# Kernel optimization log

Measured on AMD Instinct MI355X. Metric: run time of the kernel, lower is better.

Reference implementation:

```python
import jax, jax.numpy as jnp
import numpy as np

HIDDEN = 2048
N_HEADS = 32
N_KV = 8
HEAD_DIM = HIDDEN // N_HEADS  # 64
GROUP = N_HEADS // N_KV       # 4
FFN = 8192
EPS = 1e-5
ROPE_BASE = 500000.0
NEG = -1e9


def rms_norm(x, w, eps=EPS):
    var = jnp.mean(x * x, axis=-1, keepdims=True)
    return x * jax.lax.rsqrt(var + eps) * w


def rope_cos_sin(position_ids):
    # inv_freq: [head_dim//2]
    inv_freq = 1.0 / (ROPE_BASE ** (jnp.arange(0, HEAD_DIM, 2, dtype=jnp.float32) / HEAD_DIM))
    freqs = position_ids.astype(jnp.float32)[:, :, None] * inv_freq[None, None, :]  # [b,s,d/2]
    emb = jnp.concatenate([freqs, freqs], axis=-1)  # [b,s,d]
    return jnp.cos(emb), jnp.sin(emb)


def rotate_half(x):
    x1, x2 = jnp.split(x, 2, axis=-1)
    return jnp.concatenate([-x2, x1], axis=-1)


def setup_inputs() -> dict:
    key = jax.random.key(0)
    ks = jax.random.split(key, 12)
    b, s = 2, 1024
    scale_h = 1.0 / np.sqrt(HIDDEN)
    scale_f = 1.0 / np.sqrt(FFN)
    hidden_states = jax.random.normal(ks[0], (b, s, HIDDEN), jnp.float32)
    causal = jnp.where(jnp.tril(jnp.ones((s, s), bool)), 0.0, NEG).astype(jnp.float32)
    attention_mask = jnp.broadcast_to(causal[None, None], (b, 1, s, s))
    position_ids = jnp.broadcast_to(jnp.arange(s, dtype=jnp.int32)[None], (b, s))
    return {
        "hidden_states": hidden_states,
        "attention_mask": attention_mask,
        "wq": jax.random.normal(ks[1], (HIDDEN, N_HEADS * HEAD_DIM), jnp.float32) * scale_h,
        "wk": jax.random.normal(ks[2], (HIDDEN, N_KV * HEAD_DIM), jnp.float32) * scale_h,
        "wv": jax.random.normal(ks[3], (HIDDEN, N_KV * HEAD_DIM), jnp.float32) * scale_h,
        "wo": jax.random.normal(ks[4], (N_HEADS * HEAD_DIM, HIDDEN), jnp.float32) * scale_h,
        "norm1_w": jnp.ones((HIDDEN,), jnp.float32),
        "norm2_w": jnp.ones((HIDDEN,), jnp.float32),
        "w_gate": jax.random.normal(ks[5], (HIDDEN, FFN), jnp.float32) * scale_h,
        "w_up": jax.random.normal(ks[6], (HIDDEN, FFN), jnp.float32) * scale_h,
        "w_down": jax.random.normal(ks[7], (FFN, HIDDEN), jnp.float32) * scale_f,
        "position_ids": position_ids,
    }


def reference(hidden_states, attention_mask, wq, wk, wv, wo, norm1_w, norm2_w,
              w_gate, w_up, w_down, position_ids):
    b, s, _ = hidden_states.shape
    residual = hidden_states
    normed = rms_norm(hidden_states, norm1_w)

    q = (normed @ wq).reshape(b, s, N_HEADS, HEAD_DIM).transpose(0, 2, 1, 3)  # [b,H,s,d]
    k = (normed @ wk).reshape(b, s, N_KV, HEAD_DIM).transpose(0, 2, 1, 3)    # [b,G,s,d]
    v = (normed @ wv).reshape(b, s, N_KV, HEAD_DIM).transpose(0, 2, 1, 3)

    cos, sin = rope_cos_sin(position_ids)  # [b,s,d]
    cos, sin = cos[:, None], sin[:, None]  # unsqueeze head dim
    q = q * cos + rotate_half(q) * sin
    k = k * cos + rotate_half(k) * sin

    # repeat_kv: [b,G,s,d] -> [b,H,s,d]
    k = jnp.repeat(k, GROUP, axis=1)
    v = jnp.repeat(v, GROUP, axis=1)

    scores = jnp.einsum('bhqd,bhkd->bhqk', q, k)
    scores = scores + attention_mask  # mask added BEFORE scaling, as in source
    attn = jax.nn.softmax(scores / np.sqrt(HEAD_DIM), axis=-1)
    ctx = jnp.einsum('bhqk,bhkd->bhqd', attn, v)
    ctx = ctx.transpose(0, 2, 1, 3).reshape(b, s, N_HEADS * HEAD_DIM)
    attn_out = ctx @ wo

    normed_ff = rms_norm(attn_out + residual, norm2_w)
    ff = (jax.nn.silu(normed_ff @ w_gate) * (normed_ff @ w_up)) @ w_down
    return attn_out + ff
```

## Files before the change

kernel.cpp:

```cpp
#include <hip/hip_runtime.h>
#include <hip/hip_bf16.h>
#include <cstddef>
#include <cstdint>

#define T_TOK   2048
#define HID     2048
#define NHEADS  32
#define NKV     8
#define HDIM    64
#define FFN_DIM 8192
#define QKV_N   3072

typedef __hip_bfloat16 bf16;
typedef __attribute__((ext_vector_type(8))) short short8;
typedef __attribute__((ext_vector_type(4))) float f32x4;
typedef __attribute__((ext_vector_type(4))) unsigned short us4;

typedef __attribute__((address_space(1))) const void cg_void;
typedef __attribute__((address_space(3))) void lds_void;

__global__ __launch_bounds__(256) void cast_transpose(const float* __restrict__ in,
                                                      bf16* __restrict__ out,
                                                      int K, int N)
{
    __shared__ bf16 t[64][65];
    const int n0 = blockIdx.x * 64, k0 = blockIdx.y * 64;
    const int tn = threadIdx.x & 63, tk = threadIdx.x >> 6;
    #pragma unroll
    for (int kk = tk; kk < 64; kk += 4)
        t[kk][tn] = __float2bfloat16(in[(size_t)(k0 + kk) * N + n0 + tn]);
    __syncthreads();
    #pragma unroll
    for (int nn = tk; nn < 64; nn += 4)
        out[(size_t)(n0 + nn) * K + k0 + tn] = t[tn][nn];
}

__global__ __launch_bounds__(256) void cast_ilv(const float* __restrict__ in,
                                                bf16* __restrict__ out,
                                                int N, int is_up)
{
    __shared__ bf16 t[64][65];
    const int n0 = blockIdx.x * 64, k0 = blockIdx.y * 64;
    const int tn = threadIdx.x & 63, tk = threadIdx.x >> 6;
    #pragma unroll
    for (int kk = tk; kk < 64; kk += 4)
        t[kk][tn] = __float2bfloat16(in[(size_t)(k0 + kk) * N + n0 + tn]);
    __syncthreads();
    #pragma unroll
    for (int nn = tk; nn < 64; nn += 4) {
        int n = n0 + nn;
        int r = ((n >> 5) << 6) + (is_up << 5) + (n & 31);
        out[(size_t)r * HID + k0 + tn] = t[tn][nn];
    }
}

__global__ __launch_bounds__(256) void rmsnorm_kernel(const float* __restrict__ x,
                                                      const float* __restrict__ w,
                                                      bf16* __restrict__ out)
{
    __shared__ float sm[4];
    const int row = blockIdx.x, tid = threadIdx.x;
    const float4* xr = (const float4*)(x + (size_t)row * HID);
    float4 a = xr[tid], b = xr[tid + 256];
    float ss = a.x*a.x + a.y*a.y + a.z*a.z + a.w*a.w
             + b.x*b.x + b.y*b.y + b.z*b.z + b.w*b.w;
    #pragma unroll
    for (int off = 32; off; off >>= 1) ss += __shfl_down(ss, off);
    if ((tid & 63) == 0) sm[tid >> 6] = ss;
    __syncthreads();
    float sc = rsqrtf((sm[0] + sm[1] + sm[2] + sm[3]) * (1.0f / HID) + 1e-5f);
    const float4* wr = (const float4*)w;
    float4 w0 = wr[tid], w1 = wr[tid + 256];
    bf16* o = out + (size_t)row * HID;
    o[tid*4+0] = __float2bfloat16(a.x * sc * w0.x);
    o[tid*4+1] = __float2bfloat16(a.y * sc * w0.y);
    o[tid*4+2] = __float2bfloat16(a.z * sc * w0.z);
    o[tid*4+3] = __float2bfloat16(a.w * sc * w0.w);
    o[1024+tid*4+0] = __float2bfloat16(b.x * sc * w1.x);
    o[1024+tid*4+1] = __float2bfloat16(b.y * sc * w1.y);
    o[1024+tid*4+2] = __float2bfloat16(b.z * sc * w1.z);
    o[1024+tid*4+3] = __float2bfloat16(b.w * sc * w1.w);
}

__global__ __launch_bounds__(256) void rmsnorm_add_kernel(const float* __restrict__ xa,
                                                          const float* __restrict__ xb,
                                                          const float* __restrict__ w,
                                                          bf16* __restrict__ out)
{
    __shared__ float sm[4];
    const int row = blockIdx.x, tid = threadIdx.x;
    const float4* ar = (const float4*)(xa + (size_t)row * HID);
    const float4* br = (const float4*)(xb + (size_t)row * HID);
    float4 a0 = ar[tid], a1 = ar[tid + 256];
    float4 b0 = br[tid], b1 = br[tid + 256];
    float4 s0, s1;
    s0.x = a0.x + b0.x; s0.y = a0.y + b0.y; s0.z = a0.z + b0.z; s0.w = a0.w + b0.w;
    s1.x = a1.x + b1.x; s1.y = a1.y + b1.y; s1.z = a1.z + b1.z; s1.w = a1.w + b1.w;
    float ss = s0.x*s0.x + s0.y*s0.y + s0.z*s0.z + s0.w*s0.w
             + s1.x*s1.x + s1.y*s1.y + s1.z*s1.z + s1.w*s1.w;
    #pragma unroll
    for (int off = 32; off; off >>= 1) ss += __shfl_down(ss, off);
    if ((tid & 63) == 0) sm[tid >> 6] = ss;
    __syncthreads();
    float sc = rsqrtf((sm[0] + sm[1] + sm[2] + sm[3]) * (1.0f / HID) + 1e-5f);
    const float4* wr = (const float4*)w;
    float4 w0 = wr[tid], w1 = wr[tid + 256];
    bf16* o = out + (size_t)row * HID;
    o[tid*4+0] = __float2bfloat16(s0.x * sc * w0.x);
    o[tid*4+1] = __float2bfloat16(s0.y * sc * w0.y);
    o[tid*4+2] = __float2bfloat16(s0.z * sc * w0.z);
    o[tid*4+3] = __float2bfloat16(s0.w * sc * w0.w);
    o[1024+tid*4+0] = __float2bfloat16(s1.x * sc * w1.x);
    o[1024+tid*4+1] = __float2bfloat16(s1.y * sc * w1.y);
    o[1024+tid*4+2] = __float2bfloat16(s1.z * sc * w1.z);
    o[1024+tid*4+3] = __float2bfloat16(s1.w * sc * w1.w);
}

template<int BN, int EPI>
__device__ __forceinline__ void gemm_body(
    const bf16* __restrict__ A, const bf16* __restrict__ Bt,
    float* __restrict__ Cf, bf16* __restrict__ Cb,
    int lda, int kbeg, int klen, int ldc, int bx, int by)
{
    constexpr int NFR   = BN / 32;
    constexpr int CALLS = 4 + NFR;
    __shared__ bf16 As[2 * 128 * 64];
    __shared__ bf16 Bs[2 * BN * 64];
    const int tid = threadIdx.x;
    const int wv = tid >> 6, ln = tid & 63;
    const int wr = wv >> 1, wc = wv & 1;
    const size_t m0 = (size_t)by * 128;
    const size_t n0 = (size_t)bx * BN;

    const int lrow = ln >> 3;
    const int lk   = (ln & 7) ^ lrow;

    const bf16* Abase = A  + (m0 + (size_t)wv*32 + lrow) * lda + kbeg + lk*8;
    const bf16* Bbase = Bt + (n0 + (size_t)wv*NFR*8 + lrow) * lda + kbeg + lk*8;
    bf16* AsW = As + wv*2048;
    bf16* BsW = Bs + wv*NFR*512;

    auto stage = [&](int p, int tk) {
        #pragma unroll
        for (int i = 0; i < 4; ++i)
            __builtin_amdgcn_global_load_lds((cg_void*)(Abase + (size_t)i*8*lda + tk),
                                             (lds_void*)(AsW + p*8192 + i*512), 16, 0, 0);
        #pragma unroll
        for (int i = 0; i < NFR; ++i)
            __builtin_amdgcn_global_load_lds((cg_void*)(Bbase + (size_t)i*8*lda + tk),
                                             (lds_void*)(BsW + p*(BN*64) + i*512), 16, 0, 0);
    };

    f32x4 acc[4][NFR] = {};
    const int nt = klen >> 6;

    stage(0, 0);
    stage(1, 64);
    asm volatile("s_waitcnt vmcnt(%0)" :: "n"(CALLS) : "memory");
    __builtin_amdgcn_sched_barrier(0);
    __builtin_amdgcn_s_barrier();

    for (int t = 0; t < nt; ++t) {
        const int p = t & 1;
        const char* Ab = (const char*)As + p * 16384;
        const char* Bb = (const char*)Bs + p * (BN * 128);

        short8 af[4][2], bfr[NFR][2];
        #pragma unroll
        for (int ks = 0; ks < 2; ++ks) {
            const int kbyte = ks*64 + (ln >> 4)*16;
            #pragma unroll
            for (int m = 0; m < 4; ++m) {
                int row = wr*64 + m*16 + (ln & 15);
                af[m][ks] = *(const short8*)(Ab + row*128 + (kbyte ^ ((row & 7) << 4)));
            }
            #pragma unroll
            for (int n = 0; n < NFR; ++n) {
                int row = wc*(BN/2) + n*16 + (ln & 15);
                bfr[n][ks] = *(const short8*)(Bb + row*128 + (kbyte ^ ((row & 7) << 4)));
            }
        }
        asm volatile("s_waitcnt lgkmcnt(0)" ::: "memory");
        __builtin_amdgcn_sched_barrier(0);
        __builtin_amdgcn_s_barrier();

        const bool more = (t + 2 < nt);
        if (more) stage(p, (t + 2) * 64);
        __builtin_amdgcn_sched_barrier(0);

        __builtin_amdgcn_s_setprio(1);
        #pragma unroll
        for (int ks = 0; ks < 2; ++ks)
            #pragma unroll
            for (int m = 0; m < 4; ++m)
                #pragma unroll
                for (int n = 0; n < NFR; ++n)
                    acc[m][n] = __builtin_amdgcn_mfma_f32_16x16x32_bf16(af[m][ks], bfr[n][ks], acc[m][n], 0, 0, 0);
        __builtin_amdgcn_s_setprio(0);

        if (more) { asm volatile("s_waitcnt vmcnt(%0)" :: "n"(CALLS) : "memory"); }
        else      { asm volatile("s_waitcnt vmcnt(0)" ::: "memory"); }
        __builtin_amdgcn_sched_barrier(0);
        __builtin_amdgcn_s_barrier();
    }

    const int cj = ln & 15, rj = ln >> 4;
    if constexpr (EPI == 4) {
        #pragma unroll
        for (int m = 0; m < 4; ++m) {
            #pragma unroll
            for (int j = 0; j < 4; ++j) {
                size_t row = m0 + wr*64 + m*16 + rj*4 + j;
                #pragma unroll
                for (int n = 0; n < 2; ++n) {
                    int col = ((int)(n0 >> 6) + wc) * 32 + n*16 + cj;
                    float g = acc[m][n][j];
                    float u = acc[m][n+2][j];
                    Cb[row * (size_t)ldc + col] =
                        __float2bfloat16(g / (1.0f + __expf(-g)) * u);
                }
            }
        }
    } else {
        #pragma unroll
        for (int m = 0; m < 4; ++m) {
            #pragma unroll
            for (int j = 0; j < 4; ++j) {
                size_t row = m0 + wr*64 + m*16 + rj*4 + j;
                #pragma unroll
                for (int n = 0; n < NFR; ++n) {
                    int col = (int)n0 + wc*(BN/2) + n*16 + cj;
                    float v = acc[m][n][j];
                    size_t off = row * (size_t)ldc + col;
                    if constexpr (EPI == 0) Cf[off] = v;
                    else if constexpr (EPI == 5) unsafeAtomicAdd(&Cf[off], v);
                }
            }
        }
    }
}

__device__ __forceinline__ void swz(int& bx, int& by) {
    const int nwg = gridDim.x * gridDim.y;
    int orig = blockIdx.y * gridDim.x + blockIdx.x;
    int wg = (orig & 7) * (nwg >> 3) + (orig >> 3);
    by = wg % gridDim.y;
    bx = wg / gridDim.y;
}

__global__ __launch_bounds__(256) void g_qkv(const bf16* __restrict__ A,
                                             const bf16* __restrict__ Bt,
                                             float* __restrict__ C) {
    int bx, by; swz(bx, by);
    gemm_body<64,0>(A, Bt, C, nullptr, HID, 0, HID, QKV_N, bx, by);
}
__global__ __launch_bounds__(256) void g_wo(const bf16* __restrict__ A,
                                            const bf16* __restrict__ Bt,
                                            float* __restrict__ C) {
    int bx, by; swz(bx, by);
    gemm_body<64,0>(A, Bt, C, nullptr, HID, 0, HID, HID, bx, by);
}
__global__ __launch_bounds__(256) void g_gateup(const bf16* __restrict__ A,
                                                const bf16* __restrict__ Bt,
                                                bf16* __restrict__ C) {
    int bx, by; swz(bx, by);
    gemm_body<128,4>(A, Bt, nullptr, C, HID, 0, HID, FFN_DIM, bx, by);
}
__global__ __launch_bounds__(256) void g_down(const bf16* __restrict__ A,
                                              const bf16* __restrict__ Bt,
                                              float* __restrict__ C) {
    int bx, by; swz(bx, by);
    gemm_body<64,5>(A, Bt, C, nullptr, FFN_DIM, blockIdx.z * 4096, 4096, HID, bx, by);
}

__global__ __launch_bounds__(256) void rope_cast(const float* __restrict__ qkv,
                                                 const int* __restrict__ pos_ids,
                                                 bf16* __restrict__ Qp,
                                                 bf16* __restrict__ Kp)
{
    const int t = blockIdx.x, tid = threadIdx.x;
    const int b = t >> 10, s = t & 1023;
    const float pos = (float)pos_ids[t];
    const float* row = qkv + (size_t)t * QKV_N;

    {
        int idx = tid * 4;
        int hq = idx >> 5, j = idx & 31;
        float xa[4], xb[4];
        *(float4*)xa = *(const float4*)(row + hq*64 + j);
        *(float4*)xb = *(const float4*)(row + hq*64 + j + 32);
        us4 o1, o2;
        #pragma unroll
        for (int jj = 0; jj < 4; ++jj) {
            float inv = exp2f(-(float)(j + jj) * 0.5916115177913804f);
            float ang = pos * inv, c, sn;
            sincosf(ang, &sn, &c);
            o1[jj] = __bfloat16_as_ushort(__float2bfloat16(xa[jj]*c - xb[jj]*sn));
            o2[jj] = __bfloat16_as_ushort(__float2bfloat16(xb[jj]*c + xa[jj]*sn));
        }
        bf16* qd = Qp + ((size_t)(b*32 + hq)*1024 + s)*64;
        *(us4*)(qd + j)      = o1;
        *(us4*)(qd + j + 32) = o2;
    }
    {
        int hk = tid >> 5, j = tid & 31;
        float a = row[2048 + hk*64 + j];
        float bb = row[2048 + hk*64 + j + 32];
        float inv = exp2f(-(float)j * 0.5916115177913804f);
        float ang = pos * inv, c, sn;
        sincosf(ang, &sn, &c);
        bf16* kd = Kp + ((size_t)(b*8 + hk)*1024 + s)*64;
        kd[j]      = __float2bfloat16(a*c - bb*sn);
        kd[j + 32] = __float2bfloat16(bb*c + a*sn);
    }
}

__global__ __launch_bounds__(256) void vt_cast(const float* __restrict__ qkv,
                                               bf16* __restrict__ Vt)
{
    __shared__ bf16 tile[64][64];
    const int s0 = blockIdx.x * 64;
    const int sec = blockIdx.y;
    const int b = sec >> 3, hk = sec & 7;
    const int tid = threadIdx.x;
    const float* base = qkv + ((size_t)(b*1024 + s0)) * QKV_N + 2560 + hk*64;
    const int srow = tid >> 2, d0 = (tid & 3) * 16;
    #pragma unroll
    for (int q = 0; q < 4; ++q) {
        float va[4];
        *(float4*)va = *(const float4*)(base + (size_t)srow * QKV_N + d0 + q*4);
        #pragma unroll
        for (int cc = 0; cc < 4; ++cc)
            tile[d0 + q*4 + cc][srow] = __float2bfloat16(va[cc]);
    }
    __syncthreads();
    const int dr = tid >> 2, sc = (tid & 3) * 16;
    bf16* od = Vt + ((size_t)sec*64 + dr)*1024 + s0 + sc;
    *(short8*)od       = *(const short8*)&tile[dr][sc];
    *(short8*)(od + 8) = *(const short8*)&tile[dr][sc + 8];
}

__global__ __launch_bounds__(256) void attn_mfma(const bf16* __restrict__ Qp,
                                                 const bf16* __restrict__ Kp,
                                                 const bf16* __restrict__ Vt,
                                                 bf16* __restrict__ ctx)
{
    __shared__ bf16 Ks[128 * 64];
    __shared__ bf16 Vs[64 * 128];
    __shared__ bf16 Ps[4 * 32 * 128];
    const int tid = threadIdx.x;
    const int w = tid >> 6, ln = tid & 63;
    const int qt = blockIdx.x, h = blockIdx.y, b = blockIdx.z;
    const int hk = h >> 2;
    const int q0 = qt * 128;

    const bf16* qsec = Qp + ((size_t)(b*32 + h)*1024 + q0 + w*32)*64;
    const bf16* ksec = Kp + ((size_t)(b*8 + hk)*1024)*64;
    const bf16* vsec = Vt + ((size_t)(b*8 + hk))*64*1024;

    short8 qf[2][2];
    #pragma unroll
    for (int f = 0; f < 2; ++f)
        #pragma unroll
        for (int kc = 0; kc < 2; ++kc)
            qf[f][kc] = *(const short8*)(qsec + (size_t)(f*16 + (ln & 15))*64 + kc*32 + (ln >> 4)*8);

    f32x4 acc_o[2][4] = {};
    f32x4 m[2], l[2];
    #pragma unroll
    for (int f = 0; f < 2; ++f)
        #pragma unroll
        for (int j = 0; j < 4; ++j) { m[f][j] = -1e30f; l[f][j] = 0.0f; }

    const int lrow = ln >> 3;
    const int lkk  = (ln & 7) ^ lrow;
    char* PsW = (char*)Ps + w * 8192;

    const int ntiles = qt + 1;
    for (int kt = 0; kt < ntiles; ++kt) {
        const int kv0 = kt * 128;
        {
            const bf16* kbase = ksec + (size_t)(kv0 + w*32 + lrow)*64 + lkk*8;
            bf16* KsW = Ks + w*2048;
            #pragma unroll
            for (int i = 0; i < 4; ++i)
                __builtin_amdgcn_global_load_lds((cg_void*)(kbase + (size_t)i*8*64),
                                                 (lds_void*)(KsW + i*512), 16, 0, 0);
        }
        {
            bf16* VsW = Vs + w*2048;
            #pragma unroll
            for (int i = 0; i < 4; ++i) {
                int d = w*16 + i*4 + (ln >> 4);
                __builtin_amdgcn_global_load_lds(
                    (cg_void*)(vsec + (size_t)d*1024 + kv0 + (((ln & 15) ^ (d & 7))*8)),
                    (lds_void*)(VsW + i*512), 16, 0, 0);
            }
        }
        __syncthreads();

        f32x4 acc_s[2][8] = {};
        #pragma unroll
        for (int c = 0; c < 8; ++c) {
            int kvr = c*16 + (ln & 15);
            const char* krow = (const char*)Ks + kvr*128;
            short8 kf0 = *(const short8*)(krow + (((ln >> 4)*16)      ^ ((kvr & 7) << 4)));
            short8 kf1 = *(const short8*)(krow + ((64 + (ln >> 4)*16) ^ ((kvr & 7) << 4)));
            #pragma unroll
            for (int f = 0; f < 2; ++f) {
                acc_s[f][c] = __builtin_amdgcn_mfma_f32_16x16x32_bf16(qf[f][0], kf0, acc_s[f][c], 0, 0, 0);
                acc_s[f][c] = __builtin_amdgcn_mfma_f32_16x16x32_bf16(qf[f][1], kf1, acc_s[f][c], 0, 0, 0);
            }
        }

        const bool diag = (kt == qt);
        f32x4 vmax[2];
        #pragma unroll
        for (int f = 0; f < 2; ++f)
            #pragma unroll
            for (int j = 0; j < 4; ++j) vmax[f][j] = -1e30f;
        #pragma unroll
        for (int f = 0; f < 2; ++f) {
            #pragma unroll
            for (int c = 0; c < 8; ++c) {
                f32x4 t = acc_s[f][c] * 0.125f;
                if (diag) {
                    int kv = kv0 + c*16 + (ln & 15);
                    int qg = q0 + w*32 + f*16 + (ln >> 4)*4;
                    #pragma unroll
                    for (int j = 0; j < 4; ++j)
                        if (kv > qg + j) t[j] = -1e30f;
                }
                acc_s[f][c] = t;
                #pragma unroll
                for (int j = 0; j < 4; ++j) vmax[f][j] = fmaxf(vmax[f][j], t[j]);
            }
            #pragma unroll
            for (int mk = 1; mk <= 8; mk <<= 1)
                #pragma unroll
                for (int j = 0; j < 4; ++j)
                    vmax[f][j] = fmaxf(vmax[f][j], __shfl_xor(vmax[f][j], mk));
        }

        #pragma unroll
        for (int f = 0; f < 2; ++f) {
            f32x4 r;
            #pragma unroll
            for (int j = 0; j < 4; ++j) {
                float mn = fmaxf(m[f][j], vmax[f][j]);
                r[j] = __expf(m[f][j] - mn);
                m[f][j] = mn;
                l[f][j] *= r[j];
            }
            #pragma unroll
            for (int df = 0; df < 4; ++df)
                #pragma unroll
                for (int j = 0; j < 4; ++j) acc_o[f][df][j] *= r[j];
        }

        f32x4 rs[2] = {};
        #pragma unroll
        for (int f = 0; f < 2; ++f) {
            #pragma unroll
            for (int c = 0; c < 8; ++c) {
                #pragma unroll
                for (int j = 0; j < 4; ++j) {
                    float p = __expf(acc_s[f][c][j] - m[f][j]);
                    rs[f][j] += p;
                    int qloc = f*16 + (ln >> 4)*4 + j;
                    int kvb  = (c*16 + (ln & 15))*2;
                    *(bf16*)(PsW + qloc*256 + (kvb ^ ((qloc & 7) << 4))) = __float2bfloat16(p);
                }
            }
            #pragma unroll
            for (int mk = 1; mk <= 8; mk <<= 1)
                #pragma unroll
                for (int j = 0; j < 4; ++j)
                    rs[f][j] += __shfl_xor(rs[f][j], mk);
            #pragma unroll
            for (int j = 0; j < 4; ++j) l[f][j] += rs[f][j];
        }

        #pragma unroll
        for (int kc = 0; kc < 4; ++kc) {
            short8 pa[2];
            #pragma unroll
            for (int f = 0; f < 2; ++f) {
                int qloc = f*16 + (ln & 15);
                pa[f] = *(const short8*)(PsW + qloc*256 + ((kc*64 + (ln >> 4)*16) ^ ((qloc & 7) << 4)));
            }
            #pragma unroll
            for (int df = 0; df < 4; ++df) {
                int dl = df*16 + (ln & 15);
                short8 vfr = *(const short8*)((const char*)Vs + dl*256 + ((kc*64 + (ln >> 4)*16) ^ ((dl & 7) << 4)));
                #pragma unroll
                for (int f = 0; f < 2; ++f)
                    acc_o[f][df] = __builtin_amdgcn_mfma_f32_16x16x32_bf16(pa[f], vfr, acc_o[f][df], 0, 0, 0);
            }
        }
        __syncthreads();
    }

    #pragma unroll
    for (int f = 0; f < 2; ++f) {
        f32x4 inv;
        #pragma unroll
        for (int j = 0; j < 4; ++j) inv[j] = 1.0f / l[f][j];
        #pragma unroll
        for (int df = 0; df < 4; ++df) {
            #pragma unroll
            for (int j = 0; j < 4; ++j) {
                int q = q0 + w*32 + f*16 + (ln >> 4)*4 + j;
                int d = df*16 + (ln & 15);
                ctx[((size_t)b*1024 + q)*HID + h*64 + d] = __float2bfloat16(acc_o[f][df][j] * inv[j]);
            }
        }
    }
}

extern "C" void kernel_launch(void* const* d_in, const int* in_sizes, int n_in,
                              void* d_out, int out_size, void* d_ws, size_t ws_size,
                              hipStream_t stream)
{
    const float* hidden = (const float*)d_in[0];
    const float* wq = (const float*)d_in[2];
    const float* wk = (const float*)d_in[3];
    const float* wv = (const float*)d_in[4];
    const float* wo = (const float*)d_in[5];
    const float* n1 = (const float*)d_in[6];
    const float* n2 = (const float*)d_in[7];
    const float* wg = (const float*)d_in[8];
    const float* wu = (const float*)d_in[9];
    const float* wd = (const float*)d_in[10];
    const int*  pos = (const int*)d_in[11];
    float* out = (float*)d_out;
    char* ws = (char*)d_ws;

    bf16* wgu_t  = (bf16*)(ws + 0);
    bf16* wd_t   = (bf16*)(ws + 67108864);
    bf16* wqkv_t = (bf16*)(ws + 100663296);
    bf16* wo_t   = (bf16*)(ws + 113246208);
    bf16* normed = (bf16*)(ws + 121634816);
    float* qkv   = (float*)(ws + 130023424);
    bf16* ctx    = (bf16*)(ws + 155189248);
    bf16* hb     = (bf16*)(ws + 130023424);
    bf16* Qp     = (bf16*)(ws + 121634816);
    bf16* Kp     = (bf16*)(ws + 163577856);
    bf16* Vt     = (bf16*)(ws + 165675008);

    cast_transpose<<<dim3(32, 32), 256, 0, stream>>>(wq, wqkv_t, 2048, 2048);
    cast_transpose<<<dim3(8, 32),  256, 0, stream>>>(wk, wqkv_t + 4194304, 2048, 512);
    cast_transpose<<<dim3(8, 32),  256, 0, stream>>>(wv, wqkv_t + 5242880, 2048, 512);
    cast_transpose<<<dim3(32, 32), 256, 0, stream>>>(wo, wo_t, 2048, 2048);
    cast_ilv<<<dim3(128, 32), 256, 0, stream>>>(wg, wgu_t, FFN_DIM, 0);
    cast_ilv<<<dim3(128, 32), 256, 0, stream>>>(wu, wgu_t, FFN_DIM, 1);
    cast_transpose<<<dim3(32, 128),256, 0, stream>>>(wd, wd_t, 8192, 2048);

    rmsnorm_kernel<<<T_TOK, 256, 0, stream>>>(hidden, n1, normed);
    g_qkv<<<dim3(QKV_N/64, T_TOK/128), 256, 0, stream>>>(normed, wqkv_t, qkv);
    rope_cast<<<T_TOK, 256, 0, stream>>>(qkv, pos, Qp, Kp);
    vt_cast<<<dim3(16, 16), 256, 0, stream>>>(qkv, Vt);
    attn_mfma<<<dim3(8, NHEADS, 2), 256, 0, stream>>>(Qp, Kp, Vt, ctx);
    g_wo<<<dim3(HID/64, T_TOK/128), 256, 0, stream>>>(ctx, wo_t, out);
    rmsnorm_add_kernel<<<T_TOK, 256, 0, stream>>>(out, hidden, n2, normed);
    g_gateup<<<dim3(16384/128, T_TOK/128), 256, 0, stream>>>(normed, wgu_t, hb);
    g_down<<<dim3(HID/64, T_TOK/128, 2), 256, 0, stream>>>(hb, wd_t, out);
}
```

Before: 539.9 us.

## Use dedicated 256x256 tile, 512-thread kernel for gate/up GEMM

Replaces the shared 128x128, 256-thread gate/up GEMM with a dedicated kernel that computes 256x256 output tiles using 8 waves, each owning a 128x64 sub-tile. Each LDS load of A and B is reused across more MFMAs, which cuts global and LDS traffic per flop for the largest GEMM in the layer. The cost is more accumulator registers (128 floats per lane) with a launch_bounds of 512,2, which risks spills or lower occupancy. The grid shrinks to 64x8 workgroups, which may leave some CUs with uneven load. The generic gemm_body loses its bf16 SwiGLU epilogue, which is now inlined in the new kernel.

```diff
diff --git a/kernel.cpp b/kernel.cpp
--- a/kernel.cpp
+++ b/kernel.cpp
@@ -119,7 +119,7 @@
 template<int BN, int EPI>
 __device__ __forceinline__ void gemm_body(
     const bf16* __restrict__ A, const bf16* __restrict__ Bt,
-    float* __restrict__ Cf, bf16* __restrict__ Cb,
+    float* __restrict__ Cf,
     int lda, int kbeg, int klen, int ldc, int bx, int by)
 {
     constexpr int NFR   = BN / 32;
@@ -205,36 +205,18 @@
     }
 
     const int cj = ln & 15, rj = ln >> 4;
-    if constexpr (EPI == 4) {
-        #pragma unroll
-        for (int m = 0; m < 4; ++m) {
-            #pragma unroll
-            for (int j = 0; j < 4; ++j) {
-                size_t row = m0 + wr*64 + m*16 + rj*4 + j;
-                #pragma unroll
-                for (int n = 0; n < 2; ++n) {
-                    int col = ((int)(n0 >> 6) + wc) * 32 + n*16 + cj;
-                    float g = acc[m][n][j];
-                    float u = acc[m][n+2][j];
-                    Cb[row * (size_t)ldc + col] =
-                        __float2bfloat16(g / (1.0f + __expf(-g)) * u);
-                }
-            }
-        }
-    } else {
-        #pragma unroll
-        for (int m = 0; m < 4; ++m) {
-            #pragma unroll
-            for (int j = 0; j < 4; ++j) {
-                size_t row = m0 + wr*64 + m*16 + rj*4 + j;
-                #pragma unroll
-                for (int n = 0; n < NFR; ++n) {
-                    int col = (int)n0 + wc*(BN/2) + n*16 + cj;
-                    float v = acc[m][n][j];
-                    size_t off = row * (size_t)ldc + col;
-                    if constexpr (EPI == 0) Cf[off] = v;
-                    else if constexpr (EPI == 5) unsafeAtomicAdd(&Cf[off], v);
-                }
+    #pragma unroll
+    for (int m = 0; m < 4; ++m) {
+        #pragma unroll
+        for (int j = 0; j < 4; ++j) {
+            size_t row = m0 + wr*64 + m*16 + rj*4 + j;
+            #pragma unroll
+            for (int n = 0; n < NFR; ++n) {
+                int col = (int)n0 + wc*(BN/2) + n*16 + cj;
+                float v = acc[m][n][j];
+                size_t off = row * (size_t)ldc + col;
+                if constexpr (EPI == 0) Cf[off] = v;
+                else if constexpr (EPI == 5) unsafeAtomicAdd(&Cf[off], v);
             }
         }
     }
@@ -252,25 +234,146 @@
                                              const bf16* __restrict__ Bt,
                                              float* __restrict__ C) {
     int bx, by; swz(bx, by);
-    gemm_body<64,0>(A, Bt, C, nullptr, HID, 0, HID, QKV_N, bx, by);
+    gemm_body<64,0>(A, Bt, C, HID, 0, HID, QKV_N, bx, by);
 }
 __global__ __launch_bounds__(256) void g_wo(const bf16* __restrict__ A,
                                             const bf16* __restrict__ Bt,
                                             float* __restrict__ C) {
     int bx, by; swz(bx, by);
-    gemm_body<64,0>(A, Bt, C, nullptr, HID, 0, HID, HID, bx, by);
-}
-__global__ __launch_bounds__(256) void g_gateup(const bf16* __restrict__ A,
-                                                const bf16* __restrict__ Bt,
-                                                bf16* __restrict__ C) {
-    int bx, by; swz(bx, by);
-    gemm_body<128,4>(A, Bt, nullptr, C, HID, 0, HID, FFN_DIM, bx, by);
+    gemm_body<64,0>(A, Bt, C, HID, 0, HID, HID, bx, by);
 }
 __global__ __launch_bounds__(256) void g_down(const bf16* __restrict__ A,
                                               const bf16* __restrict__ Bt,
                                               float* __restrict__ C) {
     int bx, by; swz(bx, by);
-    gemm_body<64,5>(A, Bt, C, nullptr, FFN_DIM, blockIdx.z * 4096, 4096, HID, bx, by);
+    gemm_body<64,5>(A, Bt, C, FFN_DIM, blockIdx.z * 4096, 4096, HID, bx, by);
+}
+
+__global__ __launch_bounds__(512, 2) void g_gateup(const bf16* __restrict__ A,
+                                                   const bf16* __restrict__ Bt,
+                                                   bf16* __restrict__ C)
+{
+    __shared__ bf16 As[2 * 256 * 64];
+    __shared__ bf16 Bs[2 * 256 * 64];
+    const int tid = threadIdx.x;
+    const int wv = tid >> 6, ln = tid & 63;
+    const int wr = wv >> 2, wc = wv & 3;
+
+    const int nwg = gridDim.x * gridDim.y;
+    int orig = blockIdx.y * gridDim.x + blockIdx.x;
+    int wg = (orig & 7) * (nwg >> 3) + (orig >> 3);
+    const int by = wg % gridDim.y, bx = wg / gridDim.y;
+    const size_t m0 = (size_t)by * 256;
+    const size_t n0 = (size_t)bx * 256;
+
+    const int lrow = ln >> 3;
+    const int lk   = (ln & 7) ^ lrow;
+
+    const bf16* Abase = A  + (m0 + (size_t)wv*32 + lrow) * HID + lk*8;
+    const bf16* Bbase = Bt + (n0 + (size_t)wv*32 + lrow) * HID + lk*8;
+    bf16* AsW = As + wv*2048;
+    bf16* BsW = Bs + wv*2048;
+
+    auto stage = [&](int p, int tk) {
+        #pragma unroll
+        for (int i = 0; i < 4; ++i)
+            __builtin_amdgcn_global_load_lds((cg_void*)(Abase + (size_t)i*8*HID + tk),
+                                             (lds_void*)(AsW + p*16384 + i*512), 16, 0, 0);
+        #pragma unroll
+        for (int i = 0; i < 4; ++i)
+            __builtin_amdgcn_global_load_lds((cg_void*)(Bbase + (size_t)i*8*HID + tk),
+                                             (lds_void*)(BsW + p*16384 + i*512), 16, 0, 0);
+    };
+
+    f32x4 acc[8][4] = {};
+    constexpr int nt = HID / 64;
+
+    stage(0, 0);
+    stage(1, 64);
+    asm volatile("s_waitcnt vmcnt(8)" ::: "memory");
+    __builtin_amdgcn_sched_barrier(0);
+    __builtin_amdgcn_s_barrier();
+
+    for (int t = 0; t < nt; ++t) {
+        const int p = t & 1;
+        const char* Ab = (const char*)As + p * 32768;
+        const char* Bb = (const char*)Bs + p * 32768;
+
+        short8 af[8], bf[4];
+        {
+            const int kbyte = (ln >> 4) * 16;
+            #pragma unroll
+            for (int m = 0; m < 8; ++m) {
+                int row = wr*128 + m*16 + (ln & 15);
+                af[m] = *(const short8*)(Ab + row*128 + (kbyte ^ ((row & 7) << 4)));
+            }
+            #pragma unroll
+            for (int n = 0; n < 4; ++n) {
+                int row = wc*64 + n*16 + (ln & 15);
+                bf[n] = *(const short8*)(Bb + row*128 + (kbyte ^ ((row & 7) << 4)));
+            }
+        }
+        asm volatile("s_waitcnt lgkmcnt(0)" ::: "memory");
+        __builtin_amdgcn_sched_barrier(0);
+        __builtin_amdgcn_s_setprio(1);
+        #pragma unroll
+        for (int m = 0; m < 8; ++m)
+            #pragma unroll
+            for (int n = 0; n < 4; ++n)
+                acc[m][n] = __builtin_amdgcn_mfma_f32_16x16x32_bf16(af[m], bf[n], acc[m][n], 0, 0, 0);
+        __builtin_amdgcn_s_setprio(0);
+        {
+            const int kbyte = 64 + (ln >> 4) * 16;
+            #pragma unroll
+            for (int m = 0; m < 8; ++m) {
+                int row = wr*128 + m*16 + (ln & 15);
+                af[m] = *(const short8*)(Ab + row*128 + (kbyte ^ ((row & 7) << 4)));
+            }
+            #pragma unroll
+            for (int n = 0; n < 4; ++n) {
+                int row = wc*64 + n*16 + (ln & 15);
+                bf[n] = *(const short8*)(Bb + row*128 + (kbyte ^ ((row & 7) << 4)));
+            }
+        }
+        asm volatile("s_waitcnt lgkmcnt(0)" ::: "memory");
+        __builtin_amdgcn_sched_barrier(0);
+        __builtin_amdgcn_s_barrier();
+
+        const bool more = (t + 2 < nt);
+        if (more) stage(p, (t + 2) * 64);
+        __builtin_amdgcn_sched_barrier(0);
+
+        __builtin_amdgcn_s_setprio(1);
+        #pragma unroll
+        for (int m = 0; m < 8; ++m)
+            #pragma unroll
+            for (int n = 0; n < 4; ++n)
+                acc[m][n] = __builtin_amdgcn_mfma_f32_16x16x32_bf16(af[m], bf[n], acc[m][n], 0, 0, 0);
+        __builtin_amdgcn_s_setprio(0);
+
+        if (more) { asm volatile("s_waitcnt vmcnt(8)" ::: "memory"); }
+        else      { asm volatile("s_waitcnt vmcnt(0)" ::: "memory"); }
+        __builtin_amdgcn_sched_barrier(0);
+        __builtin_amdgcn_s_barrier();
+    }
+
+    const int cj = ln & 15, rj = ln >> 4;
+    const int slab = (int)(n0 >> 6) + wc;
+    #pragma unroll
+    for (int m = 0; m < 8; ++m) {
+        #pragma unroll
+        for (int j = 0; j < 4; ++j) {
+            size_t row = m0 + wr*128 + m*16 + rj*4 + j;
+            #pragma unroll
+            for (int n = 0; n < 2; ++n) {
+                int col = slab*32 + n*16 + cj;
+                float g = acc[m][n][j];
+                float u = acc[m][n+2][j];
+                C[row * (size_t)FFN_DIM + col] =
+                    __float2bfloat16(g / (1.0f + __expf(-g)) * u);
+            }
+        }
+    }
 }
 
 __global__ __launch_bounds__(256) void rope_cast(const float* __restrict__ qkv,
@@ -563,6 +666,6 @@
     attn_mfma<<<dim3(8, NHEADS, 2), 256, 0, stream>>>(Qp, Kp, Vt, ctx);
     g_wo<<<dim3(HID/64, T_TOK/128), 256, 0, stream>>>(ctx, wo_t, out);
     rmsnorm_add_kernel<<<T_TOK, 256, 0, stream>>>(out, hidden, n2, normed);
-    g_gateup<<<dim3(16384/128, T_TOK/128), 256, 0, stream>>>(normed, wgu_t, hb);
+    g_gateup<<<dim3(16384/256, T_TOK/256), 512, 0, stream>>>(normed, wgu_t, hb);
     g_down<<<dim3(HID/64, T_TOK/128, 2), 256, 0, stream>>>(hb, wd_t, out);
 }
```

Result: faster. 515.1 us (-4.6%).
